# Optimization experiments

Measured on AMD Instinct MI355X. Metric: run time of the kernel, lower is better.

The kernel has to match this reference:

```python
import jax, jax.numpy as jnp
import numpy as np

N, DIM, T, V = 32, 256, 120, 25
H, HD = 8, 32            # num_heads, head_dim
MAX_HOP = 4
SCALE = HD ** -0.5


def setup_inputs() -> dict:
    key = jax.random.key(0)
    ks = jax.random.split(key, 9)
    x = jax.random.normal(ks[0], (N, DIM, T, V), jnp.float32)
    e = jax.random.normal(ks[1], (N, DIM, T, V), jnp.float32)
    # 1x1 conv weights (trunc_normal std=0.02 in the original init)
    W_kv = jax.random.normal(ks[2], (2 * DIM, DIM), jnp.float32) * 0.02
    W_q = jax.random.normal(ks[3], (DIM, DIM), jnp.float32) * 0.02
    W_proj = jax.random.normal(ks[4], (DIM, DIM), jnp.float32) * 0.02
    b_proj = jnp.zeros((DIM,), jnp.float32)
    rpe = jax.random.normal(ks[5], (MAX_HOP + 1, DIM), jnp.float32) * 0.02
    w1 = jax.random.normal(ks[6], (H, HD), jnp.float32) * 0.02
    # outer initialized as per-head identity (plus noise so grads are interesting)
    outer = jnp.broadcast_to(jnp.eye(V, dtype=jnp.float32), (H, V, V)) \
        + 0.1 * jax.random.normal(ks[7], (H, V, V), jnp.float32)
    alpha = 0.1 * jax.random.normal(ks[8], (1,), jnp.float32)
    idx = jnp.arange(V)
    hops = jnp.minimum(jnp.abs(idx[:, None] - idx[None, :]), MAX_HOP).astype(jnp.int32)
    return dict(x=x, e=e, W_kv=W_kv, W_q=W_q, W_proj=W_proj, b_proj=b_proj,
                rpe=rpe, w1=w1, outer=outer, alpha=alpha, hops=hops)


def reference(x, e, W_kv, W_q, W_proj, b_proj, rpe, w1, outer, alpha, hops):
    n, c, t, v = x.shape
    # 1x1 convs == channel matmuls
    kv = jnp.einsum('nctv,dc->ndtv', x, W_kv)                    # [N,2*DIM,T,V]
    kv = kv.reshape(n, 2, H, HD, t, v).transpose(1, 0, 4, 2, 5, 3)  # [2,N,T,H,V,HD]
    k, vv = kv[0], kv[1]
    q = jnp.einsum('nctv,dc->ndtv', x, W_q)
    q = q.reshape(n, H, HD, t, v).transpose(0, 3, 1, 4, 2)       # [N,T,H,V,HD]
    # content score
    attn = jnp.einsum('bthnc,bthmc->bthnm', q, k)                # [N,T,H,V,V]
    # hop relative-position bias
    k_r = rpe[hops].reshape(v, v, H, HD)                         # [V,V,H,HD]
    attn = attn + jnp.einsum('bthnc,nmhc->bthnm', q, k_r)
    # group term
    e_k = e.reshape(n, H, HD, t, v).transpose(0, 3, 1, 4, 2)     # [N,T,H,V,HD]
    attn = attn + jnp.einsum('bthnc,bthmc->bthnm', q, e_k)
    # group bias (broadcast over query index)
    attn = attn + jnp.einsum('hc,bthmc->bthm', w1, e_k)[..., None, :]
    attn = jax.nn.softmax(attn * SCALE, axis=-1)
    # outer/adjacency fusion then weighted V
    out = jnp.einsum('bthnm,bthmc->bthnc', alpha[0] * attn + outer, vv)
    # [N,T,H,V,HD] -> [N,T,H,HD,V] -> [N,T,DIM,V] -> [N,DIM,T,V]
    out = out.transpose(0, 1, 2, 4, 3).reshape(n, t, H * HD, v).transpose(0, 2, 1, 3)
    out = jnp.einsum('nctv,dc->ndtv', out, W_proj) + b_proj[None, :, None, None]
    return out
```

## Files before the change

### kernel.cpp

```cpp
#include <hip/hip_runtime.h>

typedef __attribute__((ext_vector_type(8))) short bf16x8;
typedef __attribute__((ext_vector_type(4))) float f32x4;
typedef unsigned short u16;
typedef unsigned int u32;

#define SCALE_ 0.17677669529663687f
#define MFMA(a,b,c) __builtin_amdgcn_mfma_f32_16x16x32_bf16(a,b,c,0,0,0)

__device__ __forceinline__ u16 f2bf(float f){
    u32 u = __float_as_uint(f);
    u = (u + 0x7FFFu + ((u >> 16) & 1u)) >> 16;
    return (u16)u;
}
__device__ __forceinline__ float bf2f(u32 h){ return __uint_as_float(h << 16); }
__device__ __forceinline__ u32 pk2(float a, float b){ return (u32)f2bf(a) | ((u32)f2bf(b) << 16); }

__device__ __forceinline__ bf16x8 frag8(uint2 p0, uint2 p1, int kg, int l15){
    const int s0 = ((kg & 1) << 5) + l15;
    const int s1 = s0 + 16;
    u32 a0 = (u32)__shfl((int)p0.x, s0, 64);
    u32 a1 = (u32)__shfl((int)p0.y, s0, 64);
    u32 a2 = (u32)__shfl((int)p0.x, s1, 64);
    u32 a3 = (u32)__shfl((int)p0.y, s1, 64);
    u32 b0 = (u32)__shfl((int)p1.x, s0, 64);
    u32 b1 = (u32)__shfl((int)p1.y, s0, 64);
    u32 b2 = (u32)__shfl((int)p1.x, s1, 64);
    u32 b3 = (u32)__shfl((int)p1.y, s1, 64);
    const bool hi = (kg >= 2);
    union { u32 u[4]; bf16x8 v; } r;
    r.u[0] = hi ? b0 : a0; r.u[1] = hi ? b1 : a1;
    r.u[2] = hi ? b2 : a2; r.u[3] = hi ? b3 : a3;
    return r.v;
}

#define O_OFF_ 263680
__global__ void prep_kernel(const float* __restrict__ Wkv, const float* __restrict__ Wq,
                            const float* __restrict__ Wproj, const float* __restrict__ rpe,
                            const float* __restrict__ w1, u16* __restrict__ wpk)
{
    int i = blockIdx.x * 256 + threadIdx.x;
    if (i < 65536)        wpk[i] = f2bf(Wq[i]);
    else if (i < 131072)  wpk[i] = f2bf(Wkv[i - 65536]);
    else if (i < 196608){
        int j = i - 131072;
        int h = j >> 13;
        int r = j & 8191;
        int coct = r >> 8;
        int hd   = (r >> 3) & 31;
        int clo  = r & 7;
        wpk[i] = f2bf(Wkv[(size_t)(256 + h*32 + hd) * 256 + coct*8 + clo]);
    }
    else if (i < 262144)  wpk[i] = f2bf(Wproj[i - 196608]);
    else if (i < 263424){
        int j = i - 262144;
        int jj = j >> 8, h = (j >> 5) & 7, hd = j & 31;
        wpk[i] = f2bf(rpe[jj*256 + h*32 + hd]);
    }
    else if (i < 263680)  wpk[i] = f2bf(w1[i - 263424]);
}

__launch_bounds__(512)
__global__ void attn_kernel(const float* __restrict__ x, const float* __restrict__ e,
                            const float* __restrict__ outer, const float* __restrict__ alpha,
                            const u16* __restrict__ wpk, u16* __restrict__ o_ws)
{
    __shared__ __align__(16) u16 smem[6656*2 + 64];
    u16* xs  = smem;
    u16* es  = smem + 6656;

    const int tid = threadIdx.x;
    const int w = tid >> 6, lane = tid & 63;
    const int l15 = lane & 15, kg = lane >> 4;
    const int wg = (blockIdx.x & 7) * 480 + (blockIdx.x >> 3);
    const int n = wg / 120, t = wg % 120;
    const float alpha0 = alpha[0];
    const f32x4 zf = {0.f, 0.f, 0.f, 0.f};

    const float* xb = x + (size_t)n*768000 + t*25;
    const float* eb = e + (size_t)n*768000 + t*25;
    for (int i = tid; i < 6400; i += 512){
        int c = i / 25, v = i - c*25;
        int a16 = ((c>>3)*26 + v)*8 + (c&7);
        xs[a16] = f2bf(xb[c*3000 + v]);
        es[a16] = f2bf(eb[c*3000 + v]);
    }
    __syncthreads();

    const int h = w;

    f32x4 cq[2][2], ck[2][2];
    #pragma unroll
    for (int i = 0; i < 2; ++i)
        #pragma unroll
        for (int j = 0; j < 2; ++j){ cq[i][j] = zf; ck[i][j] = zf; }
    {
        const u16* wq0 = wpk + (size_t)(h*32 + l15)*256;
        const u16* wk0 = wpk + 65536 + (size_t)(h*32 + l15)*256;
        #pragma unroll
        for (int ks = 0; ks < 8; ++ks){
            bf16x8 b0 = *(const bf16x8*)&xs[((ks*4+kg)*26 + l15)*8];
            bf16x8 b1 = *(const bf16x8*)&xs[((ks*4+kg)*26 + 16 + l15)*8];
            bf16x8 aq0 = *(const bf16x8*)(wq0 + ks*32 + kg*8);
            bf16x8 aq1 = *(const bf16x8*)(wq0 + 4096 + ks*32 + kg*8);
            bf16x8 ak0 = *(const bf16x8*)(wk0 + ks*32 + kg*8);
            bf16x8 ak1 = *(const bf16x8*)(wk0 + 4096 + ks*32 + kg*8);
            cq[0][0]=MFMA(aq0,b0,cq[0][0]); cq[0][1]=MFMA(aq0,b1,cq[0][1]);
            cq[1][0]=MFMA(aq1,b0,cq[1][0]); cq[1][1]=MFMA(aq1,b1,cq[1][1]);
            ck[0][0]=MFMA(ak0,b0,ck[0][0]); ck[0][1]=MFMA(ak0,b1,ck[0][1]);
            ck[1][0]=MFMA(ak1,b0,ck[1][0]); ck[1][1]=MFMA(ak1,b1,ck[1][1]);
        }
    }
    uint2 P_q[2][2], P_k[2][2];
    #pragma unroll
    for (int mt = 0; mt < 2; ++mt)
        #pragma unroll
        for (int nt = 0; nt < 2; ++nt){
            int coct = h*4 + mt*2 + (kg>>1);
            uint2 ev = *(const uint2*)&es[(coct*26 + nt*16 + l15)*8 + (kg&1)*4];
            ck[mt][nt][0] += bf2f(ev.x & 0xFFFFu);
            ck[mt][nt][1] += bf2f(ev.x >> 16);
            ck[mt][nt][2] += bf2f(ev.y & 0xFFFFu);
            ck[mt][nt][3] += bf2f(ev.y >> 16);
            uint2 pq; pq.x = pk2(cq[mt][nt][0], cq[mt][nt][1]);
            pq.y = pk2(cq[mt][nt][2], cq[mt][nt][3]);
            P_q[nt][mt] = pq;
            uint2 pk; pk.x = pk2(ck[mt][nt][0], ck[mt][nt][1]);
            pk.y = pk2(ck[mt][nt][2], ck[mt][nt][3]);
            P_k[nt][mt] = pk;
        }

    float bias01[2];
    {
        bf16x8 aw1 = *(const bf16x8*)(wpk + 263424 + h*32 + kg*8);
        bf16x8 be0 = *(const bf16x8*)&es[((h*4+kg)*26 + l15)*8];
        bf16x8 be1 = *(const bf16x8*)&es[((h*4+kg)*26 + 16 + l15)*8];
        f32x4 cb0 = MFMA(aw1, be0, zf);
        f32x4 cb1 = MFMA(aw1, be1, zf);
        bias01[0] = cb0[0]; bias01[1] = cb1[0];
    }

    f32x4 cv[2][2];
    #pragma unroll
    for (int i = 0; i < 2; ++i)
        #pragma unroll
        for (int j = 0; j < 2; ++j) cv[i][j] = zf;
    {
        const u16* wvt = wpk + 131072 + h*8192;
        #pragma unroll
        for (int ks = 0; ks < 8; ++ks){
            bf16x8 a0 = *(const bf16x8*)&xs[((ks*4+kg)*26 + l15)*8];
            bf16x8 a1 = *(const bf16x8*)&xs[((ks*4+kg)*26 + 16 + l15)*8];
            bf16x8 bv0 = *(const bf16x8*)&wvt[((ks*4+kg)*32 + l15)*8];
            bf16x8 bv1 = *(const bf16x8*)&wvt[((ks*4+kg)*32 + 16 + l15)*8];
            cv[0][0]=MFMA(a0,bv0,cv[0][0]); cv[0][1]=MFMA(a0,bv1,cv[0][1]);
            cv[1][0]=MFMA(a1,bv0,cv[1][0]); cv[1][1]=MFMA(a1,bv1,cv[1][1]);
        }
    }
    #pragma unroll
    for (int nt = 0; nt < 2; ++nt)
        #pragma unroll
        for (int r = 0; r < 4; ++r)
            cv[1][nt][r] = (kg*4 + r < 9) ? cv[1][nt][r] : 0.f;

    uint2 P_v[2][2];
    #pragma unroll
    for (int mt = 0; mt < 2; ++mt)
        #pragma unroll
        for (int nt = 0; nt < 2; ++nt){
            uint2 pv; pv.x = pk2(cv[mt][nt][0], cv[mt][nt][1]);
            pv.y = pk2(cv[mt][nt][2], cv[mt][nt][3]);
            P_v[nt][mt] = pv;
        }

    bf16x8 fq0  = frag8(P_q[0][0], P_q[0][1], kg, l15);
    bf16x8 fq1  = frag8(P_q[1][0], P_q[1][1], kg, l15);
    bf16x8 fke0 = frag8(P_k[0][0], P_k[0][1], kg, l15);
    bf16x8 fke1 = frag8(P_k[1][0], P_k[1][1], kg, l15);
    if (l15 >= 9){
        if (l15 <= 13)
            fke1 = *(const bf16x8*)(wpk + 262144 + ((l15-9)*8 + h)*32 + kg*8);
        else {
            union { u32 u[4]; bf16x8 v; } z; z.u[0]=z.u[1]=z.u[2]=z.u[3]=0;
            fke1 = z.v;
        }
    }
    f32x4 sc[2][2];
    sc[0][0] = MFMA(fke0, fq0, zf);
    sc[0][1] = MFMA(fke0, fq1, zf);
    sc[1][0] = MFMA(fke1, fq0, zf);
    sc[1][1] = MFMA(fke1, fq1, zf);

    uint2 P_G[2][2];
    #pragma unroll
    for (int nt = 0; nt < 2; ++nt){
        const int a = nt*16 + l15;
        f32x4 s0 = sc[0][nt], s1 = sc[1][nt];
        float rr0 = __shfl(s1[1], 32 + l15, 64);
        float rr1 = __shfl(s1[2], 32 + l15, 64);
        float rr2 = __shfl(s1[3], 32 + l15, 64);
        float rr3 = __shfl(s1[0], 48 + l15, 64);
        float rr4 = __shfl(s1[1], 48 + l15, 64);
        float tv[8];
        #pragma unroll
        for (int mt = 0; mt < 2; ++mt)
            #pragma unroll
            for (int r = 0; r < 4; ++r){
                int b = mt*16 + kg*4 + r;
                float sval = mt ? s1[r] : s0[r];
                float bb = __shfl(bias01[mt], (lane & 48) + (b & 15), 64);
                int d = a - b; d = d < 0 ? -d : d; if (d > 4) d = 4;
                float rj = d==0?rr0 : d==1?rr1 : d==2?rr2 : d==3?rr3 : rr4;
                float tt = (sval + rj + bb) * SCALE_;
                tv[mt*4+r] = (b < 25) ? tt : -1e30f;
            }
        float m = tv[0];
        #pragma unroll
        for (int i = 1; i < 8; ++i) m = fmaxf(m, tv[i]);
        m = fmaxf(m, __shfl_xor(m, 16, 64));
        m = fmaxf(m, __shfl_xor(m, 32, 64));
        float ex[8], sm = 0.f;
        #pragma unroll
        for (int i = 0; i < 8; ++i){ ex[i] = __expf(tv[i] - m); sm += ex[i]; }
        sm += __shfl_xor(sm, 16, 64);
        sm += __shfl_xor(sm, 32, 64);
        const float inv = alpha0 / sm;
        float g[8];
        #pragma unroll
        for (int mt = 0; mt < 2; ++mt)
            #pragma unroll
            for (int r = 0; r < 4; ++r){
                int b = mt*16 + kg*4 + r;
                float ov = (a < 25 && b < 25) ? outer[((size_t)h*25 + a)*25 + b] : 0.f;
                g[mt*4+r] = (b < 25) ? ex[mt*4+r]*inv + ov : 0.f;
            }
        uint2 pg0; pg0.x = pk2(g[0], g[1]); pg0.y = pk2(g[2], g[3]);
        uint2 pg1; pg1.x = pk2(g[4], g[5]); pg1.y = pk2(g[6], g[7]);
        P_G[nt][0] = pg0; P_G[nt][1] = pg1;
    }

    {
        bf16x8 fv0 = frag8(P_v[0][0], P_v[0][1], kg, l15);
        bf16x8 fv1 = frag8(P_v[1][0], P_v[1][1], kg, l15);
        bf16x8 fg0 = frag8(P_G[0][0], P_G[0][1], kg, l15);
        bf16x8 fg1 = frag8(P_G[1][0], P_G[1][1], kg, l15);
        f32x4 o[2][2];
        o[0][0] = MFMA(fv0, fg0, zf); o[0][1] = MFMA(fv0, fg1, zf);
        o[1][0] = MFMA(fv1, fg0, zf); o[1][1] = MFMA(fv1, fg1, zf);
        u16* od = o_ws + (size_t)wg * 6400;
        #pragma unroll
        for (int mt = 0; mt < 2; ++mt)
            #pragma unroll
            for (int nt = 0; nt < 2; ++nt){
                int a = nt*16 + l15;
                if (a < 25){
                    int coct = h*4 + mt*2 + (kg>>1);
                    u32* dst = (u32*)&od[(coct*25 + a)*8 + (kg&1)*4];
                    dst[0] = pk2(o[mt][nt][0], o[mt][nt][1]);
                    dst[1] = pk2(o[mt][nt][2], o[mt][nt][3]);
                }
            }
    }
}

__launch_bounds__(512)
__global__ void proj_kernel(const u16* __restrict__ wpk, const u16* __restrict__ o_ws,
                            const float* __restrict__ bproj, float* __restrict__ out)
{
    const int tid = threadIdx.x;
    const int w = tid >> 6, lane = tid & 63;
    const int l15 = lane & 15, kg = lane >> 4;
    const int wg = (blockIdx.x & 7) * 480 + (blockIdx.x >> 3);
    const int n = wg / 120, t = wg % 120;
    const f32x4 zf = {0.f, 0.f, 0.f, 0.f};
    const u16* ob = o_ws + (size_t)wg * 6400;

    f32x4 pc[2][2];
    #pragma unroll
    for (int i = 0; i < 2; ++i){ pc[i][0] = zf; pc[i][1] = zf; }
    #pragma unroll
    for (int ks = 0; ks < 8; ++ks){
        bf16x8 pb0 = *(const bf16x8*)&ob[((ks*4+kg)*25 + l15)*8];
        bf16x8 pb1 = *(const bf16x8*)&ob[((ks*4+kg)*25 + 16 + l15)*8];
        #pragma unroll
        for (int i = 0; i < 2; ++i){
            bf16x8 aw = *(const bf16x8*)(wpk + 196608 +
                            (size_t)(w*32 + i*16 + l15)*256 + ks*32 + kg*8);
            pc[i][0] = MFMA(aw, pb0, pc[i][0]);
            pc[i][1] = MFMA(aw, pb1, pc[i][1]);
        }
    }
    #pragma unroll
    for (int i = 0; i < 2; ++i){
        const int d = w*32 + i*16 + kg*4;
        float b0 = bproj[d], b1 = bproj[d+1], b2 = bproj[d+2], b3 = bproj[d+3];
        #pragma unroll
        for (int nt = 0; nt < 2; ++nt){
            int v = nt*16 + l15;
            if (v < 25){
                float* op = out + (size_t)n*768000 + (size_t)d*3000 + t*25 + v;
                op[0]    = pc[i][nt][0] + b0;
                op[3000] = pc[i][nt][1] + b1;
                op[6000] = pc[i][nt][2] + b2;
                op[9000] = pc[i][nt][3] + b3;
            }
        }
    }
}

__launch_bounds__(512, 4)
__global__ void mhsa_main(const float* __restrict__ x, const float* __restrict__ e,
                          const float* __restrict__ outer, const float* __restrict__ alpha,
                          const float* __restrict__ bproj, const u16* __restrict__ wpk,
                          float* __restrict__ out)
{
    __shared__ __align__(16) u16 smem[6656*3 + 64];
    u16* xs  = smem;
    u16* es  = smem + 6656;
    u16* opk = smem + 13312;

    const int tid = threadIdx.x;
    const int w = tid >> 6, lane = tid & 63;
    const int l15 = lane & 15, kg = lane >> 4;
    const int wg = (blockIdx.x & 7) * 480 + (blockIdx.x >> 3);
    const int n = wg / 120, t = wg % 120;
    const float alpha0 = alpha[0];
    const f32x4 zf = {0.f, 0.f, 0.f, 0.f};

    const float* xb = x + (size_t)n*768000 + t*25;
    const float* eb = e + (size_t)n*768000 + t*25;
    for (int i = tid; i < 6400; i += 512){
        int c = i / 25, v = i - c*25;
        int a16 = ((c>>3)*26 + v)*8 + (c&7);
        xs[a16] = f2bf(xb[c*3000 + v]);
        es[a16] = f2bf(eb[c*3000 + v]);
    }
    __syncthreads();

    {
        const int h = w;
        f32x4 cq[2][2], ck[2][2];
        #pragma unroll
        for (int i = 0; i < 2; ++i)
            #pragma unroll
            for (int j = 0; j < 2; ++j){ cq[i][j] = zf; ck[i][j] = zf; }
        {
            const u16* wq0 = wpk + (size_t)(h*32 + l15)*256;
            const u16* wk0 = wpk + 65536 + (size_t)(h*32 + l15)*256;
            #pragma unroll
            for (int ks = 0; ks < 8; ++ks){
                bf16x8 b0 = *(const bf16x8*)&xs[((ks*4+kg)*26 + l15)*8];
                bf16x8 b1 = *(const bf16x8*)&xs[((ks*4+kg)*26 + 16 + l15)*8];
                bf16x8 aq0 = *(const bf16x8*)(wq0 + ks*32 + kg*8);
                bf16x8 aq1 = *(const bf16x8*)(wq0 + 4096 + ks*32 + kg*8);
                bf16x8 ak0 = *(const bf16x8*)(wk0 + ks*32 + kg*8);
                bf16x8 ak1 = *(const bf16x8*)(wk0 + 4096 + ks*32 + kg*8);
                cq[0][0]=MFMA(aq0,b0,cq[0][0]); cq[0][1]=MFMA(aq0,b1,cq[0][1]);
                cq[1][0]=MFMA(aq1,b0,cq[1][0]); cq[1][1]=MFMA(aq1,b1,cq[1][1]);
                ck[0][0]=MFMA(ak0,b0,ck[0][0]); ck[0][1]=MFMA(ak0,b1,ck[0][1]);
                ck[1][0]=MFMA(ak1,b0,ck[1][0]); ck[1][1]=MFMA(ak1,b1,ck[1][1]);
            }
        }
        uint2 P_q[2][2], P_k[2][2];
        #pragma unroll
        for (int mt = 0; mt < 2; ++mt)
            #pragma unroll
            for (int nt = 0; nt < 2; ++nt){
                int coct = h*4 + mt*2 + (kg>>1);
                uint2 ev = *(const uint2*)&es[(coct*26 + nt*16 + l15)*8 + (kg&1)*4];
                ck[mt][nt][0] += bf2f(ev.x & 0xFFFFu);
                ck[mt][nt][1] += bf2f(ev.x >> 16);
                ck[mt][nt][2] += bf2f(ev.y & 0xFFFFu);
                ck[mt][nt][3] += bf2f(ev.y >> 16);
                uint2 pq; pq.x = pk2(cq[mt][nt][0], cq[mt][nt][1]);
                pq.y = pk2(cq[mt][nt][2], cq[mt][nt][3]);
                P_q[nt][mt] = pq;
                uint2 pk; pk.x = pk2(ck[mt][nt][0], ck[mt][nt][1]);
                pk.y = pk2(ck[mt][nt][2], ck[mt][nt][3]);
                P_k[nt][mt] = pk;
            }
        float bias01[2];
        {
            bf16x8 aw1 = *(const bf16x8*)(wpk + 263424 + h*32 + kg*8);
            bf16x8 be0 = *(const bf16x8*)&es[((h*4+kg)*26 + l15)*8];
            bf16x8 be1 = *(const bf16x8*)&es[((h*4+kg)*26 + 16 + l15)*8];
            f32x4 cb0 = MFMA(aw1, be0, zf);
            f32x4 cb1 = MFMA(aw1, be1, zf);
            bias01[0] = cb0[0]; bias01[1] = cb1[0];
        }
        f32x4 cv[2][2];
        #pragma unroll
        for (int i = 0; i < 2; ++i)
            #pragma unroll
            for (int j = 0; j < 2; ++j) cv[i][j] = zf;
        {
            const u16* wvt = wpk + 131072 + h*8192;
            #pragma unroll
            for (int ks = 0; ks < 8; ++ks){
                bf16x8 a0 = *(const bf16x8*)&xs[((ks*4+kg)*26 + l15)*8];
                bf16x8 a1 = *(const bf16x8*)&xs[((ks*4+kg)*26 + 16 + l15)*8];
                bf16x8 bv0 = *(const bf16x8*)&wvt[((ks*4+kg)*32 + l15)*8];
                bf16x8 bv1 = *(const bf16x8*)&wvt[((ks*4+kg)*32 + 16 + l15)*8];
                cv[0][0]=MFMA(a0,bv0,cv[0][0]); cv[0][1]=MFMA(a0,bv1,cv[0][1]);
                cv[1][0]=MFMA(a1,bv0,cv[1][0]); cv[1][1]=MFMA(a1,bv1,cv[1][1]);
            }
        }
        #pragma unroll
        for (int nt = 0; nt < 2; ++nt)
            #pragma unroll
            for (int r = 0; r < 4; ++r)
                cv[1][nt][r] = (kg*4 + r < 9) ? cv[1][nt][r] : 0.f;
        uint2 P_v[2][2];
        #pragma unroll
        for (int mt = 0; mt < 2; ++mt)
            #pragma unroll
            for (int nt = 0; nt < 2; ++nt){
                uint2 pv; pv.x = pk2(cv[mt][nt][0], cv[mt][nt][1]);
                pv.y = pk2(cv[mt][nt][2], cv[mt][nt][3]);
                P_v[nt][mt] = pv;
            }
        bf16x8 fq0  = frag8(P_q[0][0], P_q[0][1], kg, l15);
        bf16x8 fq1  = frag8(P_q[1][0], P_q[1][1], kg, l15);
        bf16x8 fke0 = frag8(P_k[0][0], P_k[0][1], kg, l15);
        bf16x8 fke1 = frag8(P_k[1][0], P_k[1][1], kg, l15);
        if (l15 >= 9){
            if (l15 <= 13)
                fke1 = *(const bf16x8*)(wpk + 262144 + ((l15-9)*8 + h)*32 + kg*8);
            else {
                union { u32 u[4]; bf16x8 v; } z; z.u[0]=z.u[1]=z.u[2]=z.u[3]=0;
                fke1 = z.v;
            }
        }
        f32x4 sc[2][2];
        sc[0][0] = MFMA(fke0, fq0, zf);
        sc[0][1] = MFMA(fke0, fq1, zf);
        sc[1][0] = MFMA(fke1, fq0, zf);
        sc[1][1] = MFMA(fke1, fq1, zf);
        uint2 P_G[2][2];
        #pragma unroll
        for (int nt = 0; nt < 2; ++nt){
            const int a = nt*16 + l15;
            f32x4 s0 = sc[0][nt], s1 = sc[1][nt];
            float rr0 = __shfl(s1[1], 32 + l15, 64);
            float rr1 = __shfl(s1[2], 32 + l15, 64);
            float rr2 = __shfl(s1[3], 32 + l15, 64);
            float rr3 = __shfl(s1[0], 48 + l15, 64);
            float rr4 = __shfl(s1[1], 48 + l15, 64);
            float tv[8];
            #pragma unroll
            for (int mt = 0; mt < 2; ++mt)
                #pragma unroll
                for (int r = 0; r < 4; ++r){
                    int b = mt*16 + kg*4 + r;
                    float sval = mt ? s1[r] : s0[r];
                    float bb = __shfl(bias01[mt], (lane & 48) + (b & 15), 64);
                    int d = a - b; d = d < 0 ? -d : d; if (d > 4) d = 4;
                    float rj = d==0?rr0 : d==1?rr1 : d==2?rr2 : d==3?rr3 : rr4;
                    float tt = (sval + rj + bb) * SCALE_;
                    tv[mt*4+r] = (b < 25) ? tt : -1e30f;
                }
            float m = tv[0];
            #pragma unroll
            for (int i = 1; i < 8; ++i) m = fmaxf(m, tv[i]);
            m = fmaxf(m, __shfl_xor(m, 16, 64));
            m = fmaxf(m, __shfl_xor(m, 32, 64));
            float ex[8], sm = 0.f;
            #pragma unroll
            for (int i = 0; i < 8; ++i){ ex[i] = __expf(tv[i] - m); sm += ex[i]; }
            sm += __shfl_xor(sm, 16, 64);
            sm += __shfl_xor(sm, 32, 64);
            const float inv = alpha0 / sm;
            float g[8];
            #pragma unroll
            for (int mt = 0; mt < 2; ++mt)
                #pragma unroll
                for (int r = 0; r < 4; ++r){
                    int b = mt*16 + kg*4 + r;
                    float ov = (a < 25 && b < 25) ? outer[((size_t)h*25 + a)*25 + b] : 0.f;
                    g[mt*4+r] = (b < 25) ? ex[mt*4+r]*inv + ov : 0.f;
                }
            uint2 pg0; pg0.x = pk2(g[0], g[1]); pg0.y = pk2(g[2], g[3]);
            uint2 pg1; pg1.x = pk2(g[4], g[5]); pg1.y = pk2(g[6], g[7]);
            P_G[nt][0] = pg0; P_G[nt][1] = pg1;
        }
        {
            bf16x8 fv0 = frag8(P_v[0][0], P_v[0][1], kg, l15);
            bf16x8 fv1 = frag8(P_v[1][0], P_v[1][1], kg, l15);
            bf16x8 fg0 = frag8(P_G[0][0], P_G[0][1], kg, l15);
            bf16x8 fg1 = frag8(P_G[1][0], P_G[1][1], kg, l15);
            f32x4 o[2][2];
            o[0][0] = MFMA(fv0, fg0, zf); o[0][1] = MFMA(fv0, fg1, zf);
            o[1][0] = MFMA(fv1, fg0, zf); o[1][1] = MFMA(fv1, fg1, zf);
            #pragma unroll
            for (int mt = 0; mt < 2; ++mt)
                #pragma unroll
                for (int nt = 0; nt < 2; ++nt){
                    int a = nt*16 + l15;
                    if (a < 25){
                        int coct = h*4 + mt*2 + (kg>>1);
                        u32* dst = (u32*)&opk[(coct*26 + a)*8 + (kg&1)*4];
                        dst[0] = pk2(o[mt][nt][0], o[mt][nt][1]);
                        dst[1] = pk2(o[mt][nt][2], o[mt][nt][3]);
                    }
                }
        }
    }
    __syncthreads();

    {
        f32x4 pc[2][2];
        #pragma unroll
        for (int i = 0; i < 2; ++i){ pc[i][0] = zf; pc[i][1] = zf; }
        #pragma unroll
        for (int ks = 0; ks < 8; ++ks){
            bf16x8 pb0 = *(const bf16x8*)&opk[((ks*4+kg)*26 + l15)*8];
            bf16x8 pb1 = *(const bf16x8*)&opk[((ks*4+kg)*26 + 16 + l15)*8];
            #pragma unroll
            for (int i = 0; i < 2; ++i){
                bf16x8 aw = *(const bf16x8*)(wpk + 196608 +
                                (size_t)(w*32 + i*16 + l15)*256 + ks*32 + kg*8);
                pc[i][0] = MFMA(aw, pb0, pc[i][0]);
                pc[i][1] = MFMA(aw, pb1, pc[i][1]);
            }
        }
        #pragma unroll
        for (int i = 0; i < 2; ++i){
            const int d = w*32 + i*16 + kg*4;
            float b0 = bproj[d], b1 = bproj[d+1], b2 = bproj[d+2], b3 = bproj[d+3];
            #pragma unroll
            for (int nt = 0; nt < 2; ++nt){
                int v = nt*16 + l15;
                if (v < 25){
                    float* op = out + (size_t)n*768000 + (size_t)d*3000 + t*25 + v;
                    op[0]    = pc[i][nt][0] + b0;
                    op[3000] = pc[i][nt][1] + b1;
                    op[6000] = pc[i][nt][2] + b2;
                    op[9000] = pc[i][nt][3] + b3;
                }
            }
        }
    }
}

extern "C" void kernel_launch(void* const* d_in, const int* in_sizes, int n_in,
                              void* d_out, int out_size, void* d_ws, size_t ws_size,
                              hipStream_t stream) {
    (void)in_sizes; (void)n_in; (void)out_size;
    const float* x     = (const float*)d_in[0];
    const float* e     = (const float*)d_in[1];
    const float* Wkv   = (const float*)d_in[2];
    const float* Wq    = (const float*)d_in[3];
    const float* Wproj = (const float*)d_in[4];
    const float* bproj = (const float*)d_in[5];
    const float* rpe   = (const float*)d_in[6];
    const float* w1    = (const float*)d_in[7];
    const float* outer = (const float*)d_in[8];
    const float* alpha = (const float*)d_in[9];
    float* out = (float*)d_out;
    u16* wpk = (u16*)d_ws;

    prep_kernel<<<1030, 256, 0, stream>>>(Wkv, Wq, Wproj, rpe, w1, wpk);

    const size_t need = (size_t)O_OFF_*2 + (size_t)3840*6400*2 + 4096;
    if (ws_size >= need){
        u16* o_ws = wpk + O_OFF_;
        attn_kernel<<<32*120, 512, 0, stream>>>(x, e, outer, alpha, wpk, o_ws);
        proj_kernel<<<32*120, 512, 0, stream>>>(wpk, o_ws, bproj, out);
    } else {
        mhsa_main<<<32*120, 512, 0, stream>>>(x, e, outer, alpha, bproj, wpk, out);
    }
}
```

Before: 315.2 us.

## Process two timesteps per block in attention kernel to reuse weight loads

Each attention block now handles two adjacent timesteps instead of one, staging both x/e slices into shared memory and reusing each loaded weight fragment (Wq, Wk, Wv) for two MFMA sets. This halves the grid and the per-timestep global weight fetches, and the combined staging loop fetches adjacent memory. In exchange the block uses twice the LDS and more registers, and with half as many blocks there may be less occupancy or parallelism.

```diff
diff --git a/kernel.cpp b/kernel.cpp
--- a/kernel.cpp
+++ b/kernel.cpp
@@ -61,193 +61,243 @@
 }
 
 __launch_bounds__(512)
-__global__ void attn_kernel(const float* __restrict__ x, const float* __restrict__ e,
-                            const float* __restrict__ outer, const float* __restrict__ alpha,
-                            const u16* __restrict__ wpk, u16* __restrict__ o_ws)
+__global__ void attn2_kernel(const float* __restrict__ x, const float* __restrict__ e,
+                             const float* __restrict__ outer, const float* __restrict__ alpha,
+                             const u16* __restrict__ wpk, u16* __restrict__ o_ws)
 {
-    __shared__ __align__(16) u16 smem[6656*2 + 64];
-    u16* xs  = smem;
-    u16* es  = smem + 6656;
+    __shared__ __align__(16) u16 smem[6656*4 + 64];
+    u16* xsA = smem;
+    u16* esA = smem + 6656;
+    u16* xsB = smem + 13312;
+    u16* esB = smem + 19968;
 
     const int tid = threadIdx.x;
     const int w = tid >> 6, lane = tid & 63;
     const int l15 = lane & 15, kg = lane >> 4;
-    const int wg = (blockIdx.x & 7) * 480 + (blockIdx.x >> 3);
-    const int n = wg / 120, t = wg % 120;
+    const int wg = (blockIdx.x & 7) * 240 + (blockIdx.x >> 3);
+    const int n = wg / 60, t0 = (wg % 60) * 2;
     const float alpha0 = alpha[0];
     const f32x4 zf = {0.f, 0.f, 0.f, 0.f};
 
-    const float* xb = x + (size_t)n*768000 + t*25;
-    const float* eb = e + (size_t)n*768000 + t*25;
+    const float* xb = x + (size_t)n*768000 + t0*25;
+    const float* eb = e + (size_t)n*768000 + t0*25;
     for (int i = tid; i < 6400; i += 512){
         int c = i / 25, v = i - c*25;
         int a16 = ((c>>3)*26 + v)*8 + (c&7);
-        xs[a16] = f2bf(xb[c*3000 + v]);
-        es[a16] = f2bf(eb[c*3000 + v]);
+        int g   = c*3000 + v;
+        xsA[a16] = f2bf(xb[g]);
+        esA[a16] = f2bf(eb[g]);
+        xsB[a16] = f2bf(xb[g + 25]);
+        esB[a16] = f2bf(eb[g + 25]);
     }
     __syncthreads();
 
     const int h = w;
-
-    f32x4 cq[2][2], ck[2][2];
-    #pragma unroll
-    for (int i = 0; i < 2; ++i)
-        #pragma unroll
-        for (int j = 0; j < 2; ++j){ cq[i][j] = zf; ck[i][j] = zf; }
+    const u16* xs_[2] = {xsA, xsB};
+    const u16* es_[2] = {esA, esB};
+
+    f32x4 cq[2][2][2];
+    #pragma unroll
+    for (int c = 0; c < 2; ++c)
+        #pragma unroll
+        for (int i = 0; i < 2; ++i)
+            #pragma unroll
+            for (int j = 0; j < 2; ++j) cq[c][i][j] = zf;
     {
         const u16* wq0 = wpk + (size_t)(h*32 + l15)*256;
+        #pragma unroll
+        for (int ks = 0; ks < 8; ++ks){
+            bf16x8 a0 = *(const bf16x8*)(wq0 + ks*32 + kg*8);
+            bf16x8 a1 = *(const bf16x8*)(wq0 + 4096 + ks*32 + kg*8);
+            #pragma unroll
+            for (int c = 0; c < 2; ++c){
+                bf16x8 b0 = *(const bf16x8*)&xs_[c][((ks*4+kg)*26 + l15)*8];
+                bf16x8 b1 = *(const bf16x8*)&xs_[c][((ks*4+kg)*26 + 16 + l15)*8];
+                cq[c][0][0]=MFMA(a0,b0,cq[c][0][0]); cq[c][0][1]=MFMA(a0,b1,cq[c][0][1]);
+                cq[c][1][0]=MFMA(a1,b0,cq[c][1][0]); cq[c][1][1]=MFMA(a1,b1,cq[c][1][1]);
+            }
+        }
+    }
+    uint2 P_q[2][2][2];
+    #pragma unroll
+    for (int c = 0; c < 2; ++c)
+        #pragma unroll
+        for (int mt = 0; mt < 2; ++mt)
+            #pragma unroll
+            for (int nt = 0; nt < 2; ++nt){
+                uint2 p; p.x = pk2(cq[c][mt][nt][0], cq[c][mt][nt][1]);
+                p.y = pk2(cq[c][mt][nt][2], cq[c][mt][nt][3]);
+                P_q[c][nt][mt] = p;
+            }
+
+    f32x4 ck[2][2][2];
+    #pragma unroll
+    for (int c = 0; c < 2; ++c)
+        #pragma unroll
+        for (int i = 0; i < 2; ++i)
+            #pragma unroll
+            for (int j = 0; j < 2; ++j) ck[c][i][j] = zf;
+    {
         const u16* wk0 = wpk + 65536 + (size_t)(h*32 + l15)*256;
         #pragma unroll
         for (int ks = 0; ks < 8; ++ks){
-            bf16x8 b0 = *(const bf16x8*)&xs[((ks*4+kg)*26 + l15)*8];
-            bf16x8 b1 = *(const bf16x8*)&xs[((ks*4+kg)*26 + 16 + l15)*8];
-            bf16x8 aq0 = *(const bf16x8*)(wq0 + ks*32 + kg*8);
-            bf16x8 aq1 = *(const bf16x8*)(wq0 + 4096 + ks*32 + kg*8);
-            bf16x8 ak0 = *(const bf16x8*)(wk0 + ks*32 + kg*8);
-            bf16x8 ak1 = *(const bf16x8*)(wk0 + 4096 + ks*32 + kg*8);
-            cq[0][0]=MFMA(aq0,b0,cq[0][0]); cq[0][1]=MFMA(aq0,b1,cq[0][1]);
-            cq[1][0]=MFMA(aq1,b0,cq[1][0]); cq[1][1]=MFMA(aq1,b1,cq[1][1]);
-            ck[0][0]=MFMA(ak0,b0,ck[0][0]); ck[0][1]=MFMA(ak0,b1,ck[0][1]);
-            ck[1][0]=MFMA(ak1,b0,ck[1][0]); ck[1][1]=MFMA(ak1,b1,ck[1][1]);
-        }
-    }
-    uint2 P_q[2][2], P_k[2][2];
-    #pragma unroll
-    for (int mt = 0; mt < 2; ++mt)
-        #pragma unroll
-        for (int nt = 0; nt < 2; ++nt){
-            int coct = h*4 + mt*2 + (kg>>1);
-            uint2 ev = *(const uint2*)&es[(coct*26 + nt*16 + l15)*8 + (kg&1)*4];
-            ck[mt][nt][0] += bf2f(ev.x & 0xFFFFu);
-            ck[mt][nt][1] += bf2f(ev.x >> 16);
-            ck[mt][nt][2] += bf2f(ev.y & 0xFFFFu);
-            ck[mt][nt][3] += bf2f(ev.y >> 16);
-            uint2 pq; pq.x = pk2(cq[mt][nt][0], cq[mt][nt][1]);
-            pq.y = pk2(cq[mt][nt][2], cq[mt][nt][3]);
-            P_q[nt][mt] = pq;
-            uint2 pk; pk.x = pk2(ck[mt][nt][0], ck[mt][nt][1]);
-            pk.y = pk2(ck[mt][nt][2], ck[mt][nt][3]);
-            P_k[nt][mt] = pk;
-        }
-
-    float bias01[2];
+            bf16x8 a0 = *(const bf16x8*)(wk0 + ks*32 + kg*8);
+            bf16x8 a1 = *(const bf16x8*)(wk0 + 4096 + ks*32 + kg*8);
+            #pragma unroll
+            for (int c = 0; c < 2; ++c){
+                bf16x8 b0 = *(const bf16x8*)&xs_[c][((ks*4+kg)*26 + l15)*8];
+                bf16x8 b1 = *(const bf16x8*)&xs_[c][((ks*4+kg)*26 + 16 + l15)*8];
+                ck[c][0][0]=MFMA(a0,b0,ck[c][0][0]); ck[c][0][1]=MFMA(a0,b1,ck[c][0][1]);
+                ck[c][1][0]=MFMA(a1,b0,ck[c][1][0]); ck[c][1][1]=MFMA(a1,b1,ck[c][1][1]);
+            }
+        }
+    }
+    uint2 P_k[2][2][2];
+    #pragma unroll
+    for (int c = 0; c < 2; ++c)
+        #pragma unroll
+        for (int mt = 0; mt < 2; ++mt)
+            #pragma unroll
+            for (int nt = 0; nt < 2; ++nt){
+                int coct = h*4 + mt*2 + (kg>>1);
+                uint2 ev = *(const uint2*)&es_[c][(coct*26 + nt*16 + l15)*8 + (kg&1)*4];
+                float k0 = ck[c][mt][nt][0] + bf2f(ev.x & 0xFFFFu);
+                float k1 = ck[c][mt][nt][1] + bf2f(ev.x >> 16);
+                float k2 = ck[c][mt][nt][2] + bf2f(ev.y & 0xFFFFu);
+                float k3 = ck[c][mt][nt][3] + bf2f(ev.y >> 16);
+                uint2 p; p.x = pk2(k0, k1); p.y = pk2(k2, k3);
+                P_k[c][nt][mt] = p;
+            }
+
+    float bias01[2][2];
     {
         bf16x8 aw1 = *(const bf16x8*)(wpk + 263424 + h*32 + kg*8);
-        bf16x8 be0 = *(const bf16x8*)&es[((h*4+kg)*26 + l15)*8];
-        bf16x8 be1 = *(const bf16x8*)&es[((h*4+kg)*26 + 16 + l15)*8];
-        f32x4 cb0 = MFMA(aw1, be0, zf);
-        f32x4 cb1 = MFMA(aw1, be1, zf);
-        bias01[0] = cb0[0]; bias01[1] = cb1[0];
-    }
-
-    f32x4 cv[2][2];
-    #pragma unroll
-    for (int i = 0; i < 2; ++i)
-        #pragma unroll
-        for (int j = 0; j < 2; ++j) cv[i][j] = zf;
+        #pragma unroll
+        for (int c = 0; c < 2; ++c){
+            bf16x8 be0 = *(const bf16x8*)&es_[c][((h*4+kg)*26 + l15)*8];
+            bf16x8 be1 = *(const bf16x8*)&es_[c][((h*4+kg)*26 + 16 + l15)*8];
+            f32x4 cb0 = MFMA(aw1, be0, zf);
+            f32x4 cb1 = MFMA(aw1, be1, zf);
+            bias01[c][0] = cb0[0]; bias01[c][1] = cb1[0];
+        }
+    }
+
+    f32x4 cv[2][2][2];
+    #pragma unroll
+    for (int c = 0; c < 2; ++c)
+        #pragma unroll
+        for (int i = 0; i < 2; ++i)
+            #pragma unroll
+            for (int j = 0; j < 2; ++j) cv[c][i][j] = zf;
     {
         const u16* wvt = wpk + 131072 + h*8192;
         #pragma unroll
         for (int ks = 0; ks < 8; ++ks){
-            bf16x8 a0 = *(const bf16x8*)&xs[((ks*4+kg)*26 + l15)*8];
-            bf16x8 a1 = *(const bf16x8*)&xs[((ks*4+kg)*26 + 16 + l15)*8];
             bf16x8 bv0 = *(const bf16x8*)&wvt[((ks*4+kg)*32 + l15)*8];
             bf16x8 bv1 = *(const bf16x8*)&wvt[((ks*4+kg)*32 + 16 + l15)*8];
-            cv[0][0]=MFMA(a0,bv0,cv[0][0]); cv[0][1]=MFMA(a0,bv1,cv[0][1]);
-            cv[1][0]=MFMA(a1,bv0,cv[1][0]); cv[1][1]=MFMA(a1,bv1,cv[1][1]);
-        }
-    }
-    #pragma unroll
-    for (int nt = 0; nt < 2; ++nt)
-        #pragma unroll
-        for (int r = 0; r < 4; ++r)
-            cv[1][nt][r] = (kg*4 + r < 9) ? cv[1][nt][r] : 0.f;
-
-    uint2 P_v[2][2];
-    #pragma unroll
-    for (int mt = 0; mt < 2; ++mt)
+            #pragma unroll
+            for (int c = 0; c < 2; ++c){
+                bf16x8 a0 = *(const bf16x8*)&xs_[c][((ks*4+kg)*26 + l15)*8];
+                bf16x8 a1 = *(const bf16x8*)&xs_[c][((ks*4+kg)*26 + 16 + l15)*8];
+                cv[c][0][0]=MFMA(a0,bv0,cv[c][0][0]); cv[c][0][1]=MFMA(a0,bv1,cv[c][0][1]);
+                cv[c][1][0]=MFMA(a1,bv0,cv[c][1][0]); cv[c][1][1]=MFMA(a1,bv1,cv[c][1][1]);
+            }
+        }
+    }
+    uint2 P_v[2][2][2];
+    #pragma unroll
+    for (int c = 0; c < 2; ++c){
+        #pragma unroll
+        for (int nt = 0; nt < 2; ++nt)
+            #pragma unroll
+            for (int r = 0; r < 4; ++r)
+                cv[c][1][nt][r] = (kg*4 + r < 9) ? cv[c][1][nt][r] : 0.f;
+        #pragma unroll
+        for (int mt = 0; mt < 2; ++mt)
+            #pragma unroll
+            for (int nt = 0; nt < 2; ++nt){
+                uint2 p; p.x = pk2(cv[c][mt][nt][0], cv[c][mt][nt][1]);
+                p.y = pk2(cv[c][mt][nt][2], cv[c][mt][nt][3]);
+                P_v[c][nt][mt] = p;
+            }
+    }
+
+    #pragma unroll
+    for (int c = 0; c < 2; ++c){
+        bf16x8 fq0  = frag8(P_q[c][0][0], P_q[c][0][1], kg, l15);
+        bf16x8 fq1  = frag8(P_q[c][1][0], P_q[c][1][1], kg, l15);
+        bf16x8 fke0 = frag8(P_k[c][0][0], P_k[c][0][1], kg, l15);
+        bf16x8 fke1 = frag8(P_k[c][1][0], P_k[c][1][1], kg, l15);
+        if (l15 >= 9){
+            if (l15 <= 13)
+                fke1 = *(const bf16x8*)(wpk + 262144 + ((l15-9)*8 + h)*32 + kg*8);
+            else {
+                union { u32 u[4]; bf16x8 v; } z; z.u[0]=z.u[1]=z.u[2]=z.u[3]=0;
+                fke1 = z.v;
+            }
+        }
+        f32x4 sc[2][2];
+        sc[0][0] = MFMA(fke0, fq0, zf);
+        sc[0][1] = MFMA(fke0, fq1, zf);
+        sc[1][0] = MFMA(fke1, fq0, zf);
+        sc[1][1] = MFMA(fke1, fq1, zf);
+
+        uint2 P_G[2][2];
         #pragma unroll
         for (int nt = 0; nt < 2; ++nt){
-            uint2 pv; pv.x = pk2(cv[mt][nt][0], cv[mt][nt][1]);
-            pv.y = pk2(cv[mt][nt][2], cv[mt][nt][3]);
-            P_v[nt][mt] = pv;
-        }
-
-    bf16x8 fq0  = frag8(P_q[0][0], P_q[0][1], kg, l15);
-    bf16x8 fq1  = frag8(P_q[1][0], P_q[1][1], kg, l15);
-    bf16x8 fke0 = frag8(P_k[0][0], P_k[0][1], kg, l15);
-    bf16x8 fke1 = frag8(P_k[1][0], P_k[1][1], kg, l15);
-    if (l15 >= 9){
-        if (l15 <= 13)
-            fke1 = *(const bf16x8*)(wpk + 262144 + ((l15-9)*8 + h)*32 + kg*8);
-        else {
-            union { u32 u[4]; bf16x8 v; } z; z.u[0]=z.u[1]=z.u[2]=z.u[3]=0;
-            fke1 = z.v;
-        }
-    }
-    f32x4 sc[2][2];
-    sc[0][0] = MFMA(fke0, fq0, zf);
-    sc[0][1] = MFMA(fke0, fq1, zf);
-    sc[1][0] = MFMA(fke1, fq0, zf);
-    sc[1][1] = MFMA(fke1, fq1, zf);
-
-    uint2 P_G[2][2];
-    #pragma unroll
-    for (int nt = 0; nt < 2; ++nt){
-        const int a = nt*16 + l15;
-        f32x4 s0 = sc[0][nt], s1 = sc[1][nt];
-        float rr0 = __shfl(s1[1], 32 + l15, 64);
-        float rr1 = __shfl(s1[2], 32 + l15, 64);
-        float rr2 = __shfl(s1[3], 32 + l15, 64);
-        float rr3 = __shfl(s1[0], 48 + l15, 64);
-        float rr4 = __shfl(s1[1], 48 + l15, 64);
-        float tv[8];
-        #pragma unroll
-        for (int mt = 0; mt < 2; ++mt)
-            #pragma unroll
-            for (int r = 0; r < 4; ++r){
-                int b = mt*16 + kg*4 + r;
-                float sval = mt ? s1[r] : s0[r];
-                float bb = __shfl(bias01[mt], (lane & 48) + (b & 15), 64);
-                int d = a - b; d = d < 0 ? -d : d; if (d > 4) d = 4;
-                float rj = d==0?rr0 : d==1?rr1 : d==2?rr2 : d==3?rr3 : rr4;
-                float tt = (sval + rj + bb) * SCALE_;
-                tv[mt*4+r] = (b < 25) ? tt : -1e30f;
-            }
-        float m = tv[0];
-        #pragma unroll
-        for (int i = 1; i < 8; ++i) m = fmaxf(m, tv[i]);
-        m = fmaxf(m, __shfl_xor(m, 16, 64));
-        m = fmaxf(m, __shfl_xor(m, 32, 64));
-        float ex[8], sm = 0.f;
-        #pragma unroll
-        for (int i = 0; i < 8; ++i){ ex[i] = __expf(tv[i] - m); sm += ex[i]; }
-        sm += __shfl_xor(sm, 16, 64);
-        sm += __shfl_xor(sm, 32, 64);
-        const float inv = alpha0 / sm;
-        float g[8];
-        #pragma unroll
-        for (int mt = 0; mt < 2; ++mt)
-            #pragma unroll
-            for (int r = 0; r < 4; ++r){
-                int b = mt*16 + kg*4 + r;
-                float ov = (a < 25 && b < 25) ? outer[((size_t)h*25 + a)*25 + b] : 0.f;
-                g[mt*4+r] = (b < 25) ? ex[mt*4+r]*inv + ov : 0.f;
-            }
-        uint2 pg0; pg0.x = pk2(g[0], g[1]); pg0.y = pk2(g[2], g[3]);
-        uint2 pg1; pg1.x = pk2(g[4], g[5]); pg1.y = pk2(g[6], g[7]);
-        P_G[nt][0] = pg0; P_G[nt][1] = pg1;
-    }
-
-    {
-        bf16x8 fv0 = frag8(P_v[0][0], P_v[0][1], kg, l15);
-        bf16x8 fv1 = frag8(P_v[1][0], P_v[1][1], kg, l15);
+            const int a = nt*16 + l15;
+            f32x4 s0 = sc[0][nt], s1 = sc[1][nt];
+            float rr0 = __shfl(s1[1], 32 + l15, 64);
+            float rr1 = __shfl(s1[2], 32 + l15, 64);
+            float rr2 = __shfl(s1[3], 32 + l15, 64);
+            float rr3 = __shfl(s1[0], 48 + l15, 64);
+            float rr4 = __shfl(s1[1], 48 + l15, 64);
+            float tv[8];
+            #pragma unroll
+            for (int mt = 0; mt < 2; ++mt)
+                #pragma unroll
+                for (int r = 0; r < 4; ++r){
+                    int b = mt*16 + kg*4 + r;
+                    float sval = mt ? s1[r] : s0[r];
+                    float bb = __shfl(bias01[c][mt], (lane & 48) + (b & 15), 64);
+                    int d = a - b; d = d < 0 ? -d : d; if (d > 4) d = 4;
+                    float rj = d==0?rr0 : d==1?rr1 : d==2?rr2 : d==3?rr3 : rr4;
+                    float tt = (sval + rj + bb) * SCALE_;
+                    tv[mt*4+r] = (b < 25) ? tt : -1e30f;
+                }
+            float m = tv[0];
+            #pragma unroll
+            for (int i = 1; i < 8; ++i) m = fmaxf(m, tv[i]);
+            m = fmaxf(m, __shfl_xor(m, 16, 64));
+            m = fmaxf(m, __shfl_xor(m, 32, 64));
+            float ex[8], sm = 0.f;
+            #pragma unroll
+            for (int i = 0; i < 8; ++i){ ex[i] = __expf(tv[i] - m); sm += ex[i]; }
+            sm += __shfl_xor(sm, 16, 64);
+            sm += __shfl_xor(sm, 32, 64);
+            const float inv = alpha0 / sm;
+            float g[8];
+            #pragma unroll
+            for (int mt = 0; mt < 2; ++mt)
+                #pragma unroll
+                for (int r = 0; r < 4; ++r){
+                    int b = mt*16 + kg*4 + r;
+                    float ov = (a < 25 && b < 25) ? outer[((size_t)h*25 + a)*25 + b] : 0.f;
+                    g[mt*4+r] = (b < 25) ? ex[mt*4+r]*inv + ov : 0.f;
+                }
+            uint2 pg0; pg0.x = pk2(g[0], g[1]); pg0.y = pk2(g[2], g[3]);
+            uint2 pg1; pg1.x = pk2(g[4], g[5]); pg1.y = pk2(g[6], g[7]);
+            P_G[nt][0] = pg0; P_G[nt][1] = pg1;
+        }
+
+        bf16x8 fv0 = frag8(P_v[c][0][0], P_v[c][0][1], kg, l15);
+        bf16x8 fv1 = frag8(P_v[c][1][0], P_v[c][1][1], kg, l15);
         bf16x8 fg0 = frag8(P_G[0][0], P_G[0][1], kg, l15);
         bf16x8 fg1 = frag8(P_G[1][0], P_G[1][1], kg, l15);
         f32x4 o[2][2];
         o[0][0] = MFMA(fv0, fg0, zf); o[0][1] = MFMA(fv0, fg1, zf);
         o[1][0] = MFMA(fv1, fg0, zf); o[1][1] = MFMA(fv1, fg1, zf);
-        u16* od = o_ws + (size_t)wg * 6400;
+        u16* od = o_ws + (size_t)(n*120 + t0 + c) * 6400;
         #pragma unroll
         for (int mt = 0; mt < 2; ++mt)
             #pragma unroll
@@ -564,7 +614,7 @@
     const size_t need = (size_t)O_OFF_*2 + (size_t)3840*6400*2 + 4096;
     if (ws_size >= need){
         u16* o_ws = wpk + O_OFF_;
-        attn_kernel<<<32*120, 512, 0, stream>>>(x, e, outer, alpha, wpk, o_ws);
+        attn2_kernel<<<32*60, 512, 0, stream>>>(x, e, outer, alpha, wpk, o_ws);
         proj_kernel<<<32*120, 512, 0, stream>>>(wpk, o_ws, bproj, out);
     } else {
         mhsa_main<<<32*120, 512, 0, stream>>>(x, e, outer, alpha, bproj, wpk, out);
```

Result: faster. 308.6 us (-2.1%).
